# Kernel tuning notes

Hardware: AMD Instinct MI355X
Metric: run time of the kernel (lower is better)

The kernel has to match this reference:

```python
import jax, jax.numpy as jnp
import numpy as np

N, E = 100000, 1600000
IN_C, DIM, OUT_C = 128, 64, 64
BN_EPS = 1e-5


def setup_inputs() -> dict:
    key = jax.random.key(0)
    ks = jax.random.split(key, 16)
    s_in = 1.0 / np.sqrt(IN_C)
    s_d = 1.0 / np.sqrt(DIM)
    inp = {
        "X": jax.random.normal(ks[0], (N, IN_C), dtype=jnp.float32),
        "X_importance": jax.random.uniform(ks[1], (N, 1), dtype=jnp.float32),
        "edge_index": jax.random.randint(ks[2], (2, E), 0, N, dtype=jnp.int32),
        "gamma": jnp.ones((IN_C,), jnp.float32),
        "beta": jnp.zeros((IN_C,), jnp.float32),
        "W1": jax.random.uniform(ks[3], (IN_C, DIM), jnp.float32, -s_in, s_in),
        "b1": jnp.zeros((DIM,), jnp.float32),
        "W2": jax.random.uniform(ks[4], (DIM, DIM), jnp.float32, -s_d, s_d),
        "b2": jnp.zeros((DIM,), jnp.float32),
        "W3": jax.random.uniform(ks[5], (DIM, DIM), jnp.float32, -s_d, s_d),
        "b3": jnp.zeros((DIM,), jnp.float32),
        "W4": jax.random.uniform(ks[6], (DIM, DIM), jnp.float32, -s_d, s_d),
        "b4": jnp.zeros((DIM,), jnp.float32),
        "W5": jax.random.uniform(ks[7], (DIM, DIM), jnp.float32, -s_d, s_d),
        "b5": jnp.zeros((DIM,), jnp.float32),
        "Wf": jax.random.uniform(ks[8], (DIM, OUT_C), jnp.float32, -s_d, s_d),
    }
    return inp


def reference(X, X_importance, edge_index, gamma, beta,
              W1, b1, W2, b2, W3, b3, W4, b4, W5, b5, Wf):
    n = X.shape[0]
    src, dst = edge_index[0], edge_index[1]

    # bn_in with batch statistics (training-mode BatchNorm1d), applied to X * importance
    x = X * X_importance
    mu = jnp.mean(x, axis=0)
    var = jnp.var(x, axis=0)  # biased variance, as torch uses for normalization
    x = (x - mu) * jax.lax.rsqrt(var + BN_EPS) * gamma + beta

    def gin_conv(h, W, b):
        # GINConv, eps=0: nn((1+eps)*h + sum_{j in N(i)} h_j), nn = Linear + Tanh
        agg = jax.ops.segment_sum(h[src], dst, num_segments=n)  # [N, d]
        return jnp.tanh((h + agg) @ W + b)

    xs = []
    h = x
    for W, b in ((W1, b1), (W2, b2), (W3, b3), (W4, b4), (W5, b5)):
        h = gin_conv(h, W, b)
        xs.append(h)
    xs.append(jnp.tanh(h @ Wf))  # fc1 (no bias) + tanh
    return jnp.concatenate(xs, axis=-1)  # [N, 5*dim + out_channels]
```

## Files before the change

kernel.cpp:

```cpp
#include <hip/hip_runtime.h>
#include <hip/hip_fp16.h>
#include <cstdint>
#include <cstddef>

#define BN_EPS 1e-5f
#define STATS_B 1024

#define NPB_SHIFT 8
#define NPB 256
#define MAXNB 512
#define P1B 256
#define P2CAP 8192

__device__ __forceinline__ float tanh_fast(float x) {
    const float e = __expf(2.f * x);
    return 1.f - 2.f / (e + 1.f);
}

__device__ __forceinline__ float4 h4_to_f4(uint2 u) {
    const __half2 h0 = *reinterpret_cast<__half2*>(&u.x);
    const __half2 h1 = *reinterpret_cast<__half2*>(&u.y);
    const float2 f0 = __half22float2(h0);
    const float2 f1 = __half22float2(h1);
    return make_float4(f0.x, f0.y, f1.x, f1.y);
}

__device__ __forceinline__ unsigned pk2(float a, float b) {
    __half2 h = __floats2half2_rn(a, b);
    return *reinterpret_cast<unsigned*>(&h);
}

__device__ __forceinline__ void store_h16(__half* o, const float* a) {
    const uint4 u0 = make_uint4(pk2(a[0], a[1]),  pk2(a[2], a[3]),
                                pk2(a[4], a[5]),  pk2(a[6], a[7]));
    const uint4 u1 = make_uint4(pk2(a[8], a[9]),  pk2(a[10], a[11]),
                                pk2(a[12], a[13]), pk2(a[14], a[15]));
    *reinterpret_cast<uint4*>(o) = u0;
    *reinterpret_cast<uint4*>(o + 8) = u1;
}

__global__ __launch_bounds__(256) void k_stats(
        const float* __restrict__ X, const float* __restrict__ imp,
        float* __restrict__ ps, float* __restrict__ pq, int n) {
    __shared__ float sm[2][8][128];
    const int t = threadIdx.x;
    const int slot = t >> 5;
    const int g4 = (t & 31) << 2;
    float4 s = make_float4(0.f, 0.f, 0.f, 0.f);
    float4 q = make_float4(0.f, 0.f, 0.f, 0.f);
    for (int r = blockIdx.x * 8 + slot; r < n; r += gridDim.x * 8) {
        const float im = imp[r];
        const float4 x = *reinterpret_cast<const float4*>(X + (size_t)r * 128 + g4);
        const float vx = x.x * im, vy = x.y * im, vz = x.z * im, vw = x.w * im;
        s.x += vx; s.y += vy; s.z += vz; s.w += vw;
        q.x = fmaf(vx, vx, q.x); q.y = fmaf(vy, vy, q.y);
        q.z = fmaf(vz, vz, q.z); q.w = fmaf(vw, vw, q.w);
    }
    sm[0][slot][g4 + 0] = s.x; sm[0][slot][g4 + 1] = s.y;
    sm[0][slot][g4 + 2] = s.z; sm[0][slot][g4 + 3] = s.w;
    sm[1][slot][g4 + 0] = q.x; sm[1][slot][g4 + 1] = q.y;
    sm[1][slot][g4 + 2] = q.z; sm[1][slot][g4 + 3] = q.w;
    __syncthreads();
    if (t < 128) {
        float ss = 0.f, qq = 0.f;
#pragma unroll
        for (int sl = 0; sl < 8; ++sl) { ss += sm[0][sl][t]; qq += sm[1][sl][t]; }
        ps[blockIdx.x * 128 + t] = ss;
        pq[blockIdx.x * 128 + t] = qq;
    }
}

__global__ __launch_bounds__(1024) void k_finalize(
        const float* __restrict__ ps, const float* __restrict__ pq,
        const float* __restrict__ gamma, const float* __restrict__ beta,
        float* __restrict__ scale, float* __restrict__ shift,
        int nblocks, float inv_n) {
    __shared__ float sm[2][8][128];
    const int t = threadIdx.x;
    const int part = t >> 7;
    const int c = t & 127;
    float s = 0.f, q = 0.f;
    for (int b = part; b < nblocks; b += 8) { s += ps[b * 128 + c]; q += pq[b * 128 + c]; }
    sm[0][part][c] = s; sm[1][part][c] = q;
    __syncthreads();
    if (t < 128) {
        float ss = 0.f, qq = 0.f;
#pragma unroll
        for (int p2 = 0; p2 < 8; ++p2) { ss += sm[0][p2][t]; qq += sm[1][p2][t]; }
        const float mu  = ss * inv_n;
        const float var = fmaf(-mu, mu, qq * inv_n);
        const float rs  = rsqrtf(var + BN_EPS);
        const float sc  = gamma[t] * rs;
        scale[t] = sc;
        shift[t] = fmaf(-mu, sc, beta[t]);
    }
}

__global__ __launch_bounds__(256) void k_p1cnt(
        const int* __restrict__ dst, int* __restrict__ gh,
        int e, int nb, int chunk) {
    __shared__ int h[MAXNB];
    const int t = threadIdx.x;
    for (int i = t; i < nb; i += 256) h[i] = 0;
    __syncthreads();
    const int beg = blockIdx.x * chunk;
    const int end = (beg + chunk < e) ? beg + chunk : e;
    if (beg < e) {
        if ((e & 3) == 0) {
            const int nv = (end - beg) >> 2;
            const int4* d4p = reinterpret_cast<const int4*>(dst + beg);
            for (int i = t; i < nv; i += 256) {
                const int4 d = d4p[i];
                atomicAdd(&h[d.x >> NPB_SHIFT], 1);
                atomicAdd(&h[d.y >> NPB_SHIFT], 1);
                atomicAdd(&h[d.z >> NPB_SHIFT], 1);
                atomicAdd(&h[d.w >> NPB_SHIFT], 1);
            }
            for (int i = beg + (nv << 2) + t; i < end; i += 256)
                atomicAdd(&h[dst[i] >> NPB_SHIFT], 1);
        } else {
            for (int i = beg + t; i < end; i += 256)
                atomicAdd(&h[dst[i] >> NPB_SHIFT], 1);
        }
    }
    __syncthreads();
    for (int i = t; i < nb; i += 256) gh[blockIdx.x * MAXNB + i] = h[i];
}

__global__ __launch_bounds__(MAXNB) void k_p1scan(
        int* __restrict__ gh, int* __restrict__ bb, int e, int nb) {
    __shared__ int sm[MAXNB];
    const int t = threadIdx.x;
    int tot = 0;
    if (t < nb)
        for (int b = 0; b < P1B; ++b) tot += gh[b * MAXNB + t];
    sm[t] = (t < nb) ? tot : 0;
    __syncthreads();
    for (int off = 1; off < MAXNB; off <<= 1) {
        int u = (t >= off) ? sm[t - off] : 0;
        __syncthreads();
        sm[t] += u;
        __syncthreads();
    }
    const int excl = sm[t] - ((t < nb) ? tot : 0);
    if (t < nb) {
        bb[t] = excl;
        int run = excl;
        for (int b = 0; b < P1B; ++b) {
            const int idx = b * MAXNB + t;
            const int tmp = gh[idx];
            gh[idx] = run;
            run += tmp;
        }
    }
    if (t == 0) bb[nb] = e;
}

__global__ __launch_bounds__(256) void k_p1scat(
        const int* __restrict__ src, const int* __restrict__ dst,
        const int* __restrict__ gh, int2* __restrict__ ebuf,
        int e, int nb, int chunk) {
    __shared__ int cur[MAXNB];
    const int t = threadIdx.x;
    for (int i = t; i < nb; i += 256) cur[i] = gh[blockIdx.x * MAXNB + i];
    __syncthreads();
    const int beg = blockIdx.x * chunk;
    const int end = (beg + chunk < e) ? beg + chunk : e;
    if (beg < e) {
        if ((e & 3) == 0) {
            const int nv = (end - beg) >> 2;
            const int4* d4p = reinterpret_cast<const int4*>(dst + beg);
            const int4* s4p = reinterpret_cast<const int4*>(src + beg);
            for (int i = t; i < nv; i += 256) {
                const int4 d = d4p[i];
                const int4 s = s4p[i];
                int q;
                q = atomicAdd(&cur[d.x >> NPB_SHIFT], 1); ebuf[q] = make_int2(s.x, d.x);
                q = atomicAdd(&cur[d.y >> NPB_SHIFT], 1); ebuf[q] = make_int2(s.y, d.y);
                q = atomicAdd(&cur[d.z >> NPB_SHIFT], 1); ebuf[q] = make_int2(s.z, d.z);
                q = atomicAdd(&cur[d.w >> NPB_SHIFT], 1); ebuf[q] = make_int2(s.w, d.w);
            }
            for (int i = beg + (nv << 2) + t; i < end; i += 256) {
                const int d = dst[i];
                const int q = atomicAdd(&cur[d >> NPB_SHIFT], 1);
                ebuf[q] = make_int2(src[i], d);
            }
        } else {
            for (int i = beg + t; i < end; i += 256) {
                const int d = dst[i];
                const int q = atomicAdd(&cur[d >> NPB_SHIFT], 1);
                ebuf[q] = make_int2(src[i], d);
            }
        }
    }
}

__global__ __launch_bounds__(256) void k_p2(
        const int2* __restrict__ ebuf, const int* __restrict__ bb,
        int* __restrict__ rowptr, int* __restrict__ csr, int* __restrict__ gcur,
        int n, int nb) {
    __shared__ int lout[P2CAP];
    __shared__ int hc[NPB];
    __shared__ int sc[NPB];
    const int b = blockIdx.x;
    const int t = threadIdx.x;
    const int nodeBase = b << NPB_SHIFT;
    const int nEnd = (nodeBase + NPB < n) ? nodeBase + NPB : n;
    const int nloc = nEnd - nodeBase;
    const int rbeg = bb[b], rend = bb[b + 1];
    const int cnt = rend - rbeg;

    hc[t] = 0;
    __syncthreads();
    for (int p = rbeg + t; p < rend; p += 256)
        atomicAdd(&hc[ebuf[p].y - nodeBase], 1);
    __syncthreads();

    const int a = hc[t];
    sc[t] = a;
    __syncthreads();
    for (int off = 1; off < 256; off <<= 1) {
        int u = (t >= off) ? sc[t - off] : 0;
        __syncthreads();
        sc[t] += u;
        __syncthreads();
    }
    const int excl = sc[t] - a;
    if (t < nloc) rowptr[nodeBase + t] = rbeg + excl;
    if (b == nb - 1 && t == 0) rowptr[n] = rend;
    hc[t] = excl;
    __syncthreads();

    if (cnt <= P2CAP) {
        for (int p = rbeg + t; p < rend; p += 256) {
            const int2 sd = ebuf[p];
            const int q = atomicAdd(&hc[sd.y - nodeBase], 1);
            lout[q] = sd.x;
        }
        __syncthreads();
        for (int i = t; i < cnt; i += 256) csr[rbeg + i] = lout[i];
    } else {
        if (t < nloc) gcur[nodeBase + t] = rbeg + excl;
        __syncthreads();
        for (int p = rbeg + t; p < rend; p += 256) {
            const int2 sd = ebuf[p];
            const int q = atomicAdd(&gcur[sd.y], 1);
            csr[q] = sd.x;
        }
    }
}

__global__ __launch_bounds__(256) void k_pregemm(
        const float* __restrict__ X, const float* __restrict__ imp,
        const float* __restrict__ scale, const float* __restrict__ shift,
        const float* __restrict__ W1, __half* __restrict__ V1, int n) {
    __shared__ float tile[64 * 129];
    __shared__ float Wl[128 * 64];
    const int t = threadIdx.x;
    for (int i = t; i < 128 * 64 / 4; i += 256)
        reinterpret_cast<float4*>(Wl)[i] = reinterpret_cast<const float4*>(W1)[i];

    const int nodeL = t >> 2, q = t & 3;
    const int node = blockIdx.x * 64 + nodeL;
    if (node < n) {
        const float im = imp[node];
#pragma unroll
        for (int j = 0; j < 8; ++j) {
            const int c = q * 4 + j * 16;
            const float4 x  = *reinterpret_cast<const float4*>(X + (size_t)node * 128 + c);
            const float4 sc = *reinterpret_cast<const float4*>(scale + c);
            const float4 sh = *reinterpret_cast<const float4*>(shift + c);
            float* tr = tile + nodeL * 129 + c;
            tr[0] = fmaf(x.x * im, sc.x, sh.x);
            tr[1] = fmaf(x.y * im, sc.y, sh.y);
            tr[2] = fmaf(x.z * im, sc.z, sh.z);
            tr[3] = fmaf(x.w * im, sc.w, sh.w);
        }
    } else {
#pragma unroll
        for (int j = 0; j < 8; ++j) {
            const int c = q * 4 + j * 16;
            float* tr = tile + nodeL * 129 + c;
            tr[0] = 0.f; tr[1] = 0.f; tr[2] = 0.f; tr[3] = 0.f;
        }
    }
    __syncthreads();

    const int j0 = q * 16;
    float acc[16];
#pragma unroll
    for (int i = 0; i < 16; ++i) acc[i] = 0.f;
#pragma unroll 4
    for (int k = 0; k < 128; ++k) {
        const float ak = tile[nodeL * 129 + k];
        const float4* w = reinterpret_cast<const float4*>(Wl + k * 64 + j0);
#pragma unroll
        for (int i = 0; i < 4; ++i) {
            const float4 wv = w[i];
            acc[4 * i + 0] = fmaf(ak, wv.x, acc[4 * i + 0]);
            acc[4 * i + 1] = fmaf(ak, wv.y, acc[4 * i + 1]);
            acc[4 * i + 2] = fmaf(ak, wv.z, acc[4 * i + 2]);
            acc[4 * i + 3] = fmaf(ak, wv.w, acc[4 * i + 3]);
        }
    }
    if (node < n)
        store_h16(V1 + (size_t)node * 64 + j0, acc);
}

__global__ __launch_bounds__(256, 8) void k_gather(
        const __half* __restrict__ Vin, const float* __restrict__ bias,
        float* __restrict__ outh,
        const int* __restrict__ rowptr, const int* __restrict__ csr, int n) {
    const int lane = threadIdx.x & 63;
    const int grp  = lane >> 4;
    const int gl4  = (lane & 15) << 2;
    const int w = blockIdx.x * 4 + (threadIdx.x >> 6);
    if (w >= n) return;

    float4 acc = make_float4(0.f, 0.f, 0.f, 0.f);
    if (grp == 0) {
        const uint2 u = *reinterpret_cast<const uint2*>(Vin + (size_t)w * 64 + gl4);
        acc = h4_to_f4(u);
    }

    const int beg = rowptr[w], end = rowptr[w + 1];
    int p = beg + grp;
    for (; p + 12 < end; p += 16) {
        const int s0 = csr[p];
        const int s1 = csr[p + 4];
        const int s2 = csr[p + 8];
        const int s3 = csr[p + 12];
        const uint2 u0 = *reinterpret_cast<const uint2*>(Vin + (size_t)s0 * 64 + gl4);
        const uint2 u1 = *reinterpret_cast<const uint2*>(Vin + (size_t)s1 * 64 + gl4);
        const uint2 u2 = *reinterpret_cast<const uint2*>(Vin + (size_t)s2 * 64 + gl4);
        const uint2 u3 = *reinterpret_cast<const uint2*>(Vin + (size_t)s3 * 64 + gl4);
        const float4 v0 = h4_to_f4(u0);
        const float4 v1 = h4_to_f4(u1);
        const float4 v2 = h4_to_f4(u2);
        const float4 v3 = h4_to_f4(u3);
        acc.x += v0.x + v1.x + v2.x + v3.x;
        acc.y += v0.y + v1.y + v2.y + v3.y;
        acc.z += v0.z + v1.z + v2.z + v3.z;
        acc.w += v0.w + v1.w + v2.w + v3.w;
    }
    for (; p < end; p += 4) {
        const int s = csr[p];
        const uint2 u = *reinterpret_cast<const uint2*>(Vin + (size_t)s * 64 + gl4);
        const float4 v = h4_to_f4(u);
        acc.x += v.x; acc.y += v.y; acc.z += v.z; acc.w += v.w;
    }

    acc.x += __shfl_xor(acc.x, 16); acc.y += __shfl_xor(acc.y, 16);
    acc.z += __shfl_xor(acc.z, 16); acc.w += __shfl_xor(acc.w, 16);
    acc.x += __shfl_xor(acc.x, 32); acc.y += __shfl_xor(acc.y, 32);
    acc.z += __shfl_xor(acc.z, 32); acc.w += __shfl_xor(acc.w, 32);

    if (grp == 0) {
        const float4 bb = *reinterpret_cast<const float4*>(bias + gl4);
        float4 r;
        r.x = tanh_fast(acc.x + bb.x);
        r.y = tanh_fast(acc.y + bb.y);
        r.z = tanh_fast(acc.z + bb.z);
        r.w = tanh_fast(acc.w + bb.w);
        *reinterpret_cast<float4*>(outh + (size_t)w * 384 + gl4) = r;
    }
}

template <bool TANH, typename OutT>
__global__ __launch_bounds__(256) void k_dense(
        const float* __restrict__ hin, int in_stride,
        const float* __restrict__ W,
        OutT* __restrict__ outp, int out_stride, int n) {
    __shared__ float tile[128 * 65];
    __shared__ float Wl[64 * 64];
    const int t = threadIdx.x;
    for (int i = t; i < 64 * 64 / 4; i += 256)
        reinterpret_cast<float4*>(Wl)[i] = reinterpret_cast<const float4*>(W)[i];

    const int base = blockIdx.x * 128;
    {
        const int nodeL = t >> 1;
        const int c0 = (t & 1) * 32;
        const int node = base + nodeL;
        if (node < n) {
#pragma unroll
            for (int i = 0; i < 8; ++i) {
                const float4 v = *reinterpret_cast<const float4*>(
                    hin + (size_t)node * in_stride + c0 + 4 * i);
                float* tr = tile + nodeL * 65 + c0 + 4 * i;
                tr[0] = v.x; tr[1] = v.y; tr[2] = v.z; tr[3] = v.w;
            }
        } else {
#pragma unroll
            for (int i = 0; i < 32; ++i) tile[nodeL * 65 + c0 + i] = 0.f;
        }
    }
    __syncthreads();

    const int q = t & 3, j0 = q * 16;
    const int np = t >> 2;
    const float* r0 = tile + (2 * np) * 65;
    const float* r1 = r0 + 65;
    float acc0[16], acc1[16];
#pragma unroll
    for (int i = 0; i < 16; ++i) { acc0[i] = 0.f; acc1[i] = 0.f; }
#pragma unroll 4
    for (int k = 0; k < 64; ++k) {
        const float a0 = r0[k];
        const float a1 = r1[k];
        const float4* wr = reinterpret_cast<const float4*>(Wl + k * 64 + j0);
#pragma unroll
        for (int i = 0; i < 4; ++i) {
            const float4 wv = wr[i];
            acc0[4 * i + 0] = fmaf(a0, wv.x, acc0[4 * i + 0]);
            acc0[4 * i + 1] = fmaf(a0, wv.y, acc0[4 * i + 1]);
            acc0[4 * i + 2] = fmaf(a0, wv.z, acc0[4 * i + 2]);
            acc0[4 * i + 3] = fmaf(a0, wv.w, acc0[4 * i + 3]);
            acc1[4 * i + 0] = fmaf(a1, wv.x, acc1[4 * i + 0]);
            acc1[4 * i + 1] = fmaf(a1, wv.y, acc1[4 * i + 1]);
            acc1[4 * i + 2] = fmaf(a1, wv.z, acc1[4 * i + 2]);
            acc1[4 * i + 3] = fmaf(a1, wv.w, acc1[4 * i + 3]);
        }
    }
#pragma unroll
    for (int m = 0; m < 2; ++m) {
        const int node = base + 2 * np + m;
        if (node >= n) continue;
        float* a = m ? acc1 : acc0;
        OutT* o = outp + (size_t)node * out_stride + j0;
        if (TANH) {
#pragma unroll
            for (int i = 0; i < 16; ++i) a[i] = tanh_fast(a[i]);
        }
        if constexpr (sizeof(OutT) == 2) {
            store_h16((__half*)o, a);
        } else {
#pragma unroll
            for (int i = 0; i < 4; ++i)
                *reinterpret_cast<float4*>((float*)o + 4 * i) =
                    make_float4(a[4 * i], a[4 * i + 1], a[4 * i + 2], a[4 * i + 3]);
        }
    }
}

extern "C" void kernel_launch(void* const* d_in, const int* in_sizes, int n_in,
                              void* d_out, int out_size, void* d_ws, size_t ws_size,
                              hipStream_t stream) {
    const float* X     = (const float*)d_in[0];
    const float* imp   = (const float*)d_in[1];
    const int*   ei    = (const int*)d_in[2];
    const float* gamma = (const float*)d_in[3];
    const float* beta  = (const float*)d_in[4];
    const float* W1 = (const float*)d_in[5];
    const float* b1 = (const float*)d_in[6];
    const float* W2 = (const float*)d_in[7];
    const float* b2 = (const float*)d_in[8];
    const float* W3 = (const float*)d_in[9];
    const float* b3 = (const float*)d_in[10];
    const float* W4 = (const float*)d_in[11];
    const float* b4 = (const float*)d_in[12];
    const float* W5 = (const float*)d_in[13];
    const float* b5 = (const float*)d_in[14];
    const float* Wf = (const float*)d_in[15];
    float* out = (float*)d_out;

    const int n = in_sizes[1];
    const int e = in_sizes[2] / 2;
    const int* src = ei;
    const int* dst = ei + e;
    const int nb = (n + NPB - 1) >> NPB_SHIFT;
    const int chunk = (((e + P1B - 1) / P1B) + 3) & ~3;

    char* p = (char*)d_ws;
    auto carve = [&](size_t bytes) { char* r = p; p += (bytes + 255) & ~(size_t)255; return r; };
    int*   gh     = (int*)carve((size_t)P1B * MAXNB * sizeof(int));
    int*   bb     = (int*)carve((size_t)(MAXNB + 1) * sizeof(int));
    int*   rowptr = (int*)carve((size_t)(n + 1) * sizeof(int));
    int*   csr    = (int*)carve((size_t)e * sizeof(int));
    int*   gcur   = (int*)carve((size_t)n * sizeof(int));
    float* ps     = (float*)carve((size_t)STATS_B * 128 * sizeof(float));
    float* pq     = (float*)carve((size_t)STATS_B * 128 * sizeof(float));
    float* scale  = (float*)carve(128 * sizeof(float));
    float* shift  = (float*)carve(128 * sizeof(float));
    char*  uni    = carve((size_t)e * sizeof(int2) > 2 * (size_t)n * 64 * sizeof(__half)
                          ? (size_t)e * sizeof(int2)
                          : 2 * (size_t)n * 64 * sizeof(__half));
    __half* VA    = (__half*)uni;
    __half* VB    = (__half*)(uni + (size_t)n * 64 * sizeof(__half));
    int2*  ebuf   = (int2*)uni;

    const int ntiles64  = (n + 63) / 64;
    const int ntiles128 = (n + 127) / 128;
    const int ngather = (n + 3) / 4;

    k_stats<<<STATS_B, 256, 0, stream>>>(X, imp, ps, pq, n);
    k_finalize<<<1, 1024, 0, stream>>>(ps, pq, gamma, beta, scale, shift, STATS_B, 1.0f / (float)n);

    k_p1cnt<<<P1B, 256, 0, stream>>>(dst, gh, e, nb, chunk);
    k_p1scan<<<1, MAXNB, 0, stream>>>(gh, bb, e, nb);
    k_p1scat<<<P1B, 256, 0, stream>>>(src, dst, gh, ebuf, e, nb, chunk);
    k_p2<<<nb, 256, 0, stream>>>(ebuf, bb, rowptr, csr, gcur, n, nb);

    k_pregemm<<<ntiles64, 256, 0, stream>>>(X, imp, scale, shift, W1, VA, n);

    k_gather<<<ngather, 256, 0, stream>>>(VA, b1, out + 0,   rowptr, csr, n);
    k_dense<false, __half><<<ntiles128, 256, 0, stream>>>(out + 0,   384, W2, VB, 64, n);
    k_gather<<<ngather, 256, 0, stream>>>(VB, b2, out + 64,  rowptr, csr, n);
    k_dense<false, __half><<<ntiles128, 256, 0, stream>>>(out + 64,  384, W3, VA, 64, n);
    k_gather<<<ngather, 256, 0, stream>>>(VA, b3, out + 128, rowptr, csr, n);
    k_dense<false, __half><<<ntiles128, 256, 0, stream>>>(out + 128, 384, W4, VB, 64, n);
    k_gather<<<ngather, 256, 0, stream>>>(VB, b4, out + 192, rowptr, csr, n);
    k_dense<false, __half><<<ntiles128, 256, 0, stream>>>(out + 192, 384, W5, VA, 64, n);
    k_gather<<<ngather, 256, 0, stream>>>(VA, b5, out + 256, rowptr, csr, n);
    k_dense<true, float><<<ntiles128, 256, 0, stream>>>(out + 256, 384, Wf, out + 320, 384, n);
}
```

Measured before the change: 511.8 us.

## Retile per-thread GEMM micro-tiles and shrink CSR bucket size

Changes the register micro-tile in the pregemm kernel from one node by 16 columns to two nodes by 8 columns. In the dense transform kernel it goes from two nodes by 16 columns to four nodes by 8 columns, so each loaded weight float4 is reused across more rows and fewer loads are spent per FMA. The CSR build now uses 128-node buckets (more blocks) with a guarded scan, and the stats grid is enlarged. The aim is better LDS reuse and more parallelism, at the cost of a different shared-memory bank access pattern and more blocks in the partitioning passes.

```diff
diff --git a/kernel.cpp b/kernel.cpp
--- a/kernel.cpp
+++ b/kernel.cpp
@@ -4,11 +4,11 @@
 #include <cstddef>
 
 #define BN_EPS 1e-5f
-#define STATS_B 1024
-
-#define NPB_SHIFT 8
-#define NPB 256
-#define MAXNB 512
+#define STATS_B 2048
+
+#define NPB_SHIFT 7
+#define NPB 128
+#define MAXNB 1024
 #define P1B 256
 #define P2CAP 8192
 
@@ -30,13 +30,10 @@
     return *reinterpret_cast<unsigned*>(&h);
 }
 
-__device__ __forceinline__ void store_h16(__half* o, const float* a) {
-    const uint4 u0 = make_uint4(pk2(a[0], a[1]),  pk2(a[2], a[3]),
-                                pk2(a[4], a[5]),  pk2(a[6], a[7]));
-    const uint4 u1 = make_uint4(pk2(a[8], a[9]),  pk2(a[10], a[11]),
-                                pk2(a[12], a[13]), pk2(a[14], a[15]));
-    *reinterpret_cast<uint4*>(o) = u0;
-    *reinterpret_cast<uint4*>(o + 8) = u1;
+__device__ __forceinline__ void store_h8(__half* o, const float* a) {
+    const uint4 u = make_uint4(pk2(a[0], a[1]), pk2(a[2], a[3]),
+                               pk2(a[4], a[5]), pk2(a[6], a[7]));
+    *reinterpret_cast<uint4*>(o) = u;
 }
 
 __global__ __launch_bounds__(256) void k_stats(
@@ -210,25 +207,25 @@
     const int rbeg = bb[b], rend = bb[b + 1];
     const int cnt = rend - rbeg;
 
-    hc[t] = 0;
+    if (t < NPB) hc[t] = 0;
     __syncthreads();
     for (int p = rbeg + t; p < rend; p += 256)
         atomicAdd(&hc[ebuf[p].y - nodeBase], 1);
     __syncthreads();
 
-    const int a = hc[t];
-    sc[t] = a;
-    __syncthreads();
-    for (int off = 1; off < 256; off <<= 1) {
-        int u = (t >= off) ? sc[t - off] : 0;
+    int a = 0;
+    if (t < NPB) { a = hc[t]; sc[t] = a; }
+    __syncthreads();
+    for (int off = 1; off < NPB; off <<= 1) {
+        int u = (t >= off && t < NPB) ? sc[t - off] : 0;
         __syncthreads();
-        sc[t] += u;
+        if (t < NPB) sc[t] += u;
         __syncthreads();
     }
-    const int excl = sc[t] - a;
+    const int excl = (t < NPB) ? sc[t] - a : 0;
     if (t < nloc) rowptr[nodeBase + t] = rbeg + excl;
     if (b == nb - 1 && t == 0) rowptr[n] = rend;
-    hc[t] = excl;
+    if (t < NPB) hc[t] = excl;
     __syncthreads();
 
     if (cnt <= P2CAP) {
@@ -260,51 +257,60 @@
     for (int i = t; i < 128 * 64 / 4; i += 256)
         reinterpret_cast<float4*>(Wl)[i] = reinterpret_cast<const float4*>(W1)[i];
 
-    const int nodeL = t >> 2, q = t & 3;
-    const int node = blockIdx.x * 64 + nodeL;
-    if (node < n) {
-        const float im = imp[node];
-#pragma unroll
-        for (int j = 0; j < 8; ++j) {
-            const int c = q * 4 + j * 16;
-            const float4 x  = *reinterpret_cast<const float4*>(X + (size_t)node * 128 + c);
-            const float4 sc = *reinterpret_cast<const float4*>(scale + c);
-            const float4 sh = *reinterpret_cast<const float4*>(shift + c);
-            float* tr = tile + nodeL * 129 + c;
-            tr[0] = fmaf(x.x * im, sc.x, sh.x);
-            tr[1] = fmaf(x.y * im, sc.y, sh.y);
-            tr[2] = fmaf(x.z * im, sc.z, sh.z);
-            tr[3] = fmaf(x.w * im, sc.w, sh.w);
-        }
-    } else {
-#pragma unroll
-        for (int j = 0; j < 8; ++j) {
-            const int c = q * 4 + j * 16;
-            float* tr = tile + nodeL * 129 + c;
-            tr[0] = 0.f; tr[1] = 0.f; tr[2] = 0.f; tr[3] = 0.f;
-        }
-    }
-    __syncthreads();
-
-    const int j0 = q * 16;
-    float acc[16];
-#pragma unroll
-    for (int i = 0; i < 16; ++i) acc[i] = 0.f;
+    {
+        const int nodeL = t >> 2, q = t & 3;
+        const int node = blockIdx.x * 64 + nodeL;
+        if (node < n) {
+            const float im = imp[node];
+#pragma unroll
+            for (int j = 0; j < 8; ++j) {
+                const int c = q * 4 + j * 16;
+                const float4 x  = *reinterpret_cast<const float4*>(X + (size_t)node * 128 + c);
+                const float4 sc = *reinterpret_cast<const float4*>(scale + c);
+                const float4 sh = *reinterpret_cast<const float4*>(shift + c);
+                float* tr = tile + nodeL * 129 + c;
+                tr[0] = fmaf(x.x * im, sc.x, sh.x);
+                tr[1] = fmaf(x.y * im, sc.y, sh.y);
+                tr[2] = fmaf(x.z * im, sc.z, sh.z);
+                tr[3] = fmaf(x.w * im, sc.w, sh.w);
+            }
+        } else {
+#pragma unroll
+            for (int j = 0; j < 8; ++j) {
+                const int c = q * 4 + j * 16;
+                float* tr = tile + nodeL * 129 + c;
+                tr[0] = 0.f; tr[1] = 0.f; tr[2] = 0.f; tr[3] = 0.f;
+            }
+        }
+    }
+    __syncthreads();
+
+    const int j0 = (t & 7) * 8;
+    const int np = t >> 3;
+    const float* r0 = tile + (2 * np) * 129;
+    float acc0[8], acc1[8];
+#pragma unroll
+    for (int i = 0; i < 8; ++i) { acc0[i] = 0.f; acc1[i] = 0.f; }
 #pragma unroll 4
     for (int k = 0; k < 128; ++k) {
-        const float ak = tile[nodeL * 129 + k];
-        const float4* w = reinterpret_cast<const float4*>(Wl + k * 64 + j0);
-#pragma unroll
-        for (int i = 0; i < 4; ++i) {
-            const float4 wv = w[i];
-            acc[4 * i + 0] = fmaf(ak, wv.x, acc[4 * i + 0]);
-            acc[4 * i + 1] = fmaf(ak, wv.y, acc[4 * i + 1]);
-            acc[4 * i + 2] = fmaf(ak, wv.z, acc[4 * i + 2]);
-            acc[4 * i + 3] = fmaf(ak, wv.w, acc[4 * i + 3]);
-        }
-    }
-    if (node < n)
-        store_h16(V1 + (size_t)node * 64 + j0, acc);
+        const float a0 = r0[k];
+        const float a1 = r0[129 + k];
+        const float4 w0 = *reinterpret_cast<const float4*>(Wl + k * 64 + j0);
+        const float4 w1 = *reinterpret_cast<const float4*>(Wl + k * 64 + j0 + 4);
+        acc0[0] = fmaf(a0, w0.x, acc0[0]); acc0[1] = fmaf(a0, w0.y, acc0[1]);
+        acc0[2] = fmaf(a0, w0.z, acc0[2]); acc0[3] = fmaf(a0, w0.w, acc0[3]);
+        acc0[4] = fmaf(a0, w1.x, acc0[4]); acc0[5] = fmaf(a0, w1.y, acc0[5]);
+        acc0[6] = fmaf(a0, w1.z, acc0[6]); acc0[7] = fmaf(a0, w1.w, acc0[7]);
+        acc1[0] = fmaf(a1, w0.x, acc1[0]); acc1[1] = fmaf(a1, w0.y, acc1[1]);
+        acc1[2] = fmaf(a1, w0.z, acc1[2]); acc1[3] = fmaf(a1, w0.w, acc1[3]);
+        acc1[4] = fmaf(a1, w1.x, acc1[4]); acc1[5] = fmaf(a1, w1.y, acc1[5]);
+        acc1[6] = fmaf(a1, w1.z, acc1[6]); acc1[7] = fmaf(a1, w1.w, acc1[7]);
+    }
+    {
+        const int n0 = blockIdx.x * 64 + 2 * np;
+        if (n0 < n)     store_h8(V1 + (size_t)n0 * 64 + j0, acc0);
+        if (n0 + 1 < n) store_h8(V1 + (size_t)(n0 + 1) * 64 + j0, acc1);
+    }
 }
 
 __global__ __launch_bounds__(256, 8) void k_gather(
@@ -397,48 +403,48 @@
     }
     __syncthreads();
 
-    const int q = t & 3, j0 = q * 16;
-    const int np = t >> 2;
-    const float* r0 = tile + (2 * np) * 65;
-    const float* r1 = r0 + 65;
-    float acc0[16], acc1[16];
-#pragma unroll
-    for (int i = 0; i < 16; ++i) { acc0[i] = 0.f; acc1[i] = 0.f; }
+    const int j0 = (t & 7) * 8;
+    const int np = t >> 3;
+    const float* r0 = tile + (4 * np) * 65;
+    float acc[4][8];
+#pragma unroll
+    for (int m = 0; m < 4; ++m)
+#pragma unroll
+        for (int i = 0; i < 8; ++i) acc[m][i] = 0.f;
 #pragma unroll 4
     for (int k = 0; k < 64; ++k) {
-        const float a0 = r0[k];
-        const float a1 = r1[k];
-        const float4* wr = reinterpret_cast<const float4*>(Wl + k * 64 + j0);
-#pragma unroll
-        for (int i = 0; i < 4; ++i) {
-            const float4 wv = wr[i];
-            acc0[4 * i + 0] = fmaf(a0, wv.x, acc0[4 * i + 0]);
-            acc0[4 * i + 1] = fmaf(a0, wv.y, acc0[4 * i + 1]);
-            acc0[4 * i + 2] = fmaf(a0, wv.z, acc0[4 * i + 2]);
-            acc0[4 * i + 3] = fmaf(a0, wv.w, acc0[4 * i + 3]);
-            acc1[4 * i + 0] = fmaf(a1, wv.x, acc1[4 * i + 0]);
-            acc1[4 * i + 1] = fmaf(a1, wv.y, acc1[4 * i + 1]);
-            acc1[4 * i + 2] = fmaf(a1, wv.z, acc1[4 * i + 2]);
-            acc1[4 * i + 3] = fmaf(a1, wv.w, acc1[4 * i + 3]);
-        }
-    }
-#pragma unroll
-    for (int m = 0; m < 2; ++m) {
-        const int node = base + 2 * np + m;
+        const float4 w0 = *reinterpret_cast<const float4*>(Wl + k * 64 + j0);
+        const float4 w1 = *reinterpret_cast<const float4*>(Wl + k * 64 + j0 + 4);
+        const float am[4] = { r0[k], r0[65 + k], r0[130 + k], r0[195 + k] };
+#pragma unroll
+        for (int m = 0; m < 4; ++m) {
+            acc[m][0] = fmaf(am[m], w0.x, acc[m][0]);
+            acc[m][1] = fmaf(am[m], w0.y, acc[m][1]);
+            acc[m][2] = fmaf(am[m], w0.z, acc[m][2]);
+            acc[m][3] = fmaf(am[m], w0.w, acc[m][3]);
+            acc[m][4] = fmaf(am[m], w1.x, acc[m][4]);
+            acc[m][5] = fmaf(am[m], w1.y, acc[m][5]);
+            acc[m][6] = fmaf(am[m], w1.z, acc[m][6]);
+            acc[m][7] = fmaf(am[m], w1.w, acc[m][7]);
+        }
+    }
+#pragma unroll
+    for (int m = 0; m < 4; ++m) {
+        const int node = base + 4 * np + m;
         if (node >= n) continue;
-        float* a = m ? acc1 : acc0;
+        float* a = acc[m];
+        if (TANH) {
+#pragma unroll
+            for (int i = 0; i < 8; ++i) a[i] = tanh_fast(a[i]);
+        }
         OutT* o = outp + (size_t)node * out_stride + j0;
-        if (TANH) {
-#pragma unroll
-            for (int i = 0; i < 16; ++i) a[i] = tanh_fast(a[i]);
-        }
         if constexpr (sizeof(OutT) == 2) {
-            store_h16((__half*)o, a);
+            store_h8((__half*)o, a);
         } else {
-#pragma unroll
-            for (int i = 0; i < 4; ++i)
-                *reinterpret_cast<float4*>((float*)o + 4 * i) =
-                    make_float4(a[4 * i], a[4 * i + 1], a[4 * i + 2], a[4 * i + 3]);
+            *reinterpret_cast<float4*>((float*)o) =
+                make_float4(a[0], a[1], a[2], a[3]);
+            *reinterpret_cast<float4*>((float*)o + 4) =
+                make_float4(a[4], a[5], a[6], a[7]);
         }
     }
 }
```

New measurement: 548.8 us. 1.07x slower.
